# Kernel optimization log

Measured on AMD Instinct MI355X. Metric: run time of the kernel, lower is better.

Reference implementation:

```python
import jax, jax.numpy as jnp
import numpy as np
from jax import lax

WINDOW_SIZE = 11
SIGMA = 1.5
C1 = 0.01 ** 2
C2 = 0.03 ** 2


def _gaussian_window(channel, window_size=WINDOW_SIZE, sigma=SIGMA, dtype=jnp.float32):
    x = jnp.arange(window_size, dtype=dtype) - window_size // 2
    g = jnp.exp(-(x ** 2) / (2.0 * sigma ** 2))
    g = g / g.sum()
    w2 = jnp.outer(g, g)  # [K, K]
    # depthwise kernel: [C_out=C, C_in/groups=1, K, K]
    return jnp.broadcast_to(w2[None, None], (channel, 1, window_size, window_size))


def _dwconv(x, window, channel, window_size=WINDOW_SIZE):
    pad = window_size // 2
    return lax.conv_general_dilated(
        x, window,
        window_strides=(1, 1),
        padding=[(pad, pad), (pad, pad)],
        dimension_numbers=('NCHW', 'OIHW', 'NCHW'),
        feature_group_count=channel,
    )


def setup_inputs() -> dict:
    key = jax.random.key(0)
    k1, k2 = jax.random.split(key)
    img1 = jax.random.uniform(k1, (16, 3, 512, 512), dtype=jnp.float32)
    img2 = jax.random.uniform(k2, (16, 3, 512, 512), dtype=jnp.float32)
    return {"img1": img1, "img2": img2}


def reference(img1, img2):
    channel = img1.shape[1]
    window = _gaussian_window(channel, dtype=img1.dtype)

    mu1 = _dwconv(img1, window, channel)
    mu2 = _dwconv(img2, window, channel)
    mu1_sq = mu1 * mu1
    mu2_sq = mu2 * mu2
    mu1_mu2 = mu1 * mu2

    sigma1_sq = _dwconv(img1 * img1, window, channel) - mu1_sq
    sigma2_sq = _dwconv(img2 * img2, window, channel) - mu2_sq
    sigma12 = _dwconv(img1 * img2, window, channel) - mu1_mu2

    ssim_map = ((2.0 * mu1_mu2 + C1) * (2.0 * sigma12 + C2)) / (
        (mu1_sq + mu2_sq + C1) * (sigma1_sq + sigma2_sq + C2))
    return ssim_map.mean()
```

## Files before the change

kernel.cpp:

```cpp
#include <hip/hip_runtime.h>

namespace {
constexpr int IMG_W = 512, IMG_H = 512;
constexpr int TW = 32, TH = 32;
constexpr int IN_W = TW + 10, IN_H = TH + 10;
constexpr int S12_STR = 46;
constexpr float C1c = 0.01f * 0.01f;
constexpr float C2c = 0.03f * 0.03f;

constexpr float GW[11] = {
    1.0283799e-03f, 7.5987582e-03f, 3.6000773e-02f, 1.0936069e-01f,
    2.1300554e-01f, 2.6601172e-01f, 2.1300554e-01f, 1.0936069e-01f,
    3.6000773e-02f, 7.5987582e-03f, 1.0283799e-03f
};

using v2f = __attribute__((ext_vector_type(2))) float;
using v4f = __attribute__((ext_vector_type(4))) float;

__device__ __forceinline__ void pkfma(v2f& acc, v2f w, v2f a) {
    asm("v_pk_fma_f32 %0, %1, %2, %0" : "+v"(acc) : "s"(w), "v"(a));
}
__device__ __forceinline__ v2f pkmul(v2f a, v2f b) {
    v2f d;
    asm("v_pk_mul_f32 %0, %1, %2" : "=v"(d) : "v"(a), "v"(b));
    return d;
}
__device__ __forceinline__ v2f bcast(float w) { v2f r; r.x = w; r.y = w; return r; }

__device__ __forceinline__ int hidx(int row, int col) {
    return row * 32 + ((col + row) & 31);
}
}

__global__ __launch_bounds__(256, 6) void ssim_tile_kernel(
        const float* __restrict__ img1, const float* __restrict__ img2,
        double* __restrict__ acc)
{
    union SharedU {
        v2f s12[IN_H * S12_STR];
        v4f h4 [IN_H * 32];
    };
    __shared__ SharedU u;
    __shared__ float wred[4];

    const int tid = threadIdx.x;
    const size_t base = (size_t)blockIdx.z * (IMG_W * IMG_H);
    const float* p1 = img1 + base;
    const float* p2 = img2 + base;
    const int x0e = blockIdx.x * TW - 6;
    const int y0  = blockIdx.y * TH - 5;

    {
        v4f* s12v4 = (v4f*)u.s12;
        int r   = tid / 22;
        int cf2 = tid - r * 22;
        int goff = (y0 + r) * IMG_W + x0e + 2 * cf2;
        int soff = r * 23 + cf2;
        const bool interior =
            blockIdx.x > 0 && blockIdx.x < gridDim.x - 1 &&
            blockIdx.y > 0 && blockIdx.y < gridDim.y - 1;
        if (interior) {
#pragma unroll
            for (int i = 0; i < 4; ++i) {
                if (i < 3 || tid < 924 - 3 * 256) {
                    const float2 a = *(const float2*)&p1[goff];
                    const float2 b = *(const float2*)&p2[goff];
                    v4f q; q.x = a.x; q.y = b.x; q.z = a.y; q.w = b.y;
                    s12v4[soff] = q;
                }
                const bool wrap = cf2 + 14 >= 22;
                cf2  += wrap ? -8 : 14;
                r    += wrap ? 12 : 11;
                goff += wrap ? 12 * IMG_W - 16 : 11 * IMG_W + 28;
                soff += wrap ? 12 * 23 - 8     : 11 * 23 + 14;
            }
        } else {
#pragma unroll
            for (int i = 0; i < 4; ++i) {
                if (i < 3 || tid < 924 - 3 * 256) {
                    const int gy = y0 + r;
                    const int gx = x0e + 2 * cf2;
                    float a0 = 0.f, a1 = 0.f, b0 = 0.f, b1 = 0.f;
                    if (gy >= 0 && gy < IMG_H) {
                        if (gx >= 0 && gx < IMG_W)         { a0 = p1[goff];     b0 = p2[goff]; }
                        if (gx + 1 >= 0 && gx + 1 < IMG_W) { a1 = p1[goff + 1]; b1 = p2[goff + 1]; }
                    }
                    v4f q; q.x = a0; q.y = b0; q.z = a1; q.w = b1;
                    s12v4[soff] = q;
                }
                const bool wrap = cf2 + 14 >= 22;
                cf2  += wrap ? -8 : 14;
                r    += wrap ? 12 : 11;
                goff += wrap ? 12 * IMG_W - 16 : 11 * IMG_W + 28;
                soff += wrap ? 12 * 23 - 8     : 11 * 23 + 14;
            }
        }
    }
    __syncthreads();

    const int r2 = tid >> 2;
    const int g2 = tid & 3;
    const int cb = g2 * 8;
    v2f mu8[8], sx8[8];
    if (tid < 168) {
#pragma unroll
        for (int j = 0; j < 8; ++j) { mu8[j] = bcast(0.f); sx8[j] = bcast(0.f); }
        const v4f* srow = (const v4f*)u.s12 + (r2 * 23 + g2 * 4);
#pragma unroll
        for (int m = 0; m < 10; ++m) {
            const v4f q = srow[m];
#pragma unroll
            for (int half = 0; half < 2; ++half) {
                const int k = 2 * m + half;
                v2f v;
                v.x = half ? q.z : q.x;
                v.y = half ? q.w : q.y;
                const v2f a2 = pkmul(v, v);
                v2f sx;
                sx.x = a2.x + a2.y;
                sx.y = v.x * v.y;
#pragma unroll
                for (int j = 0; j < 8; ++j) {
                    const int t = k - j - 1;
                    if (t >= 0 && t < 11) {
                        const v2f w2 = bcast(GW[t]);
                        pkfma(mu8[j], w2, v);
                        pkfma(sx8[j], w2, sx);
                    }
                }
            }
        }
    }
    __syncthreads();
    if (tid < 168) {
#pragma unroll
        for (int j = 0; j < 8; ++j) {
            v4f q;
            q.x = mu8[j].x; q.y = mu8[j].y;
            q.z = sx8[j].x; q.w = sx8[j].y;
            u.h4[hidx(r2, cb + j)] = q;
        }
    }
    __syncthreads();

    const int c3 = tid & 31;
    const int rb = (tid >> 5) * 4;
    v2f mu4[4], sx4[4];
#pragma unroll
    for (int j = 0; j < 4; ++j) { mu4[j] = bcast(0.f); sx4[j] = bcast(0.f); }
#pragma unroll
    for (int k = 0; k < 14; ++k) {
        const v4f q = u.h4[hidx(rb + k, c3)];
        v2f hm; hm.x = q.x; hm.y = q.y;
        v2f hx; hx.x = q.z; hx.y = q.w;
#pragma unroll
        for (int j = 0; j < 4; ++j) {
            const int t = k - j;
            if (t >= 0 && t < 11) {
                const v2f w2 = bcast(GW[t]);
                pkfma(mu4[j], w2, hm);
                pkfma(sx4[j], w2, hx);
            }
        }
    }
    float lsum = 0.f;
#pragma unroll
    for (int j = 0; j < 4; ++j) {
        const v2f musq = pkmul(mu4[j], mu4[j]);
        const float mu12 = mu4[j].x * mu4[j].y;
        const float sden = musq.x + musq.y;
        const float s12v = sx4[j].y - mu12;
        const float ssum = sx4[j].x - sden;
        const float num = (2.f * mu12 + C1c) * (2.f * s12v + C2c);
        const float den = (sden + C1c) * (ssum + C2c);
        lsum += __fdividef(num, den);
    }

#pragma unroll
    for (int off = 32; off > 0; off >>= 1)
        lsum += __shfl_down(lsum, off, 64);
    if ((tid & 63) == 0) wred[tid >> 6] = lsum;
    __syncthreads();
    if (tid == 0) {
        const int bid = (blockIdx.z * gridDim.y + blockIdx.y) * gridDim.x + blockIdx.x;
        unsafeAtomicAdd(&acc[bid & 255],
                        (double)(wred[0] + wred[1] + wred[2] + wred[3]));
    }
}

__global__ __launch_bounds__(256) void ssim_final_kernel(
        const double* __restrict__ acc, float* __restrict__ out, double inv_total)
{
    const int tid = threadIdx.x;
    double a = acc[tid];
#pragma unroll
    for (int off = 32; off > 0; off >>= 1)
        a += __shfl_down(a, off, 64);
    __shared__ double ws[4];
    if ((tid & 63) == 0) ws[tid >> 6] = a;
    __syncthreads();
    if (tid == 0)
        out[0] = (float)((ws[0] + ws[1] + ws[2] + ws[3]) * inv_total);
}

extern "C" void kernel_launch(void* const* d_in, const int* in_sizes, int n_in,
                              void* d_out, int out_size, void* d_ws, size_t ws_size,
                              hipStream_t stream)
{
    const float* img1 = (const float*)d_in[0];
    const float* img2 = (const float*)d_in[1];
    double* acc = (double*)d_ws;

    hipMemsetAsync(d_ws, 0, 256 * sizeof(double), stream);

    const int nch = in_sizes[0] / (IMG_W * IMG_H);
    dim3 grid(IMG_W / TW, IMG_H / TH, nch);
    ssim_tile_kernel<<<grid, 256, 0, stream>>>(img1, img2, acc);

    const double inv_total = 1.0 / (double)in_sizes[0];
    ssim_final_kernel<<<1, 256, 0, stream>>>(acc, (float*)d_out, inv_total);
}
```

Baseline: 152.1 us.

## Double tile height to 64 rows and share one swizzled LDS plane

```diff
diff --git a/kernel.cpp b/kernel.cpp
--- a/kernel.cpp
+++ b/kernel.cpp
@@ -2,9 +2,10 @@
 
 namespace {
 constexpr int IMG_W = 512, IMG_H = 512;
-constexpr int TW = 32, TH = 32;
-constexpr int IN_W = TW + 10, IN_H = TH + 10;
-constexpr int S12_STR = 46;
+constexpr int TW = 32, TH = 64;
+constexpr int IN_H = TH + 10;
+constexpr int IN_UNITS = 22;
+constexpr int P1_TASKS = IN_H * IN_UNITS;
 constexpr float C1c = 0.01f * 0.01f;
 constexpr float C2c = 0.03f * 0.03f;
 
@@ -27,20 +28,16 @@
 }
 __device__ __forceinline__ v2f bcast(float w) { v2f r; r.x = w; r.y = w; return r; }
 
-__device__ __forceinline__ int hidx(int row, int col) {
+__device__ __forceinline__ int pidx(int row, int col) {
     return row * 32 + ((col + row) & 31);
 }
 }
 
-__global__ __launch_bounds__(256, 6) void ssim_tile_kernel(
+__global__ __launch_bounds__(256, 4) void ssim_tile_kernel(
         const float* __restrict__ img1, const float* __restrict__ img2,
         double* __restrict__ acc)
 {
-    union SharedU {
-        v2f s12[IN_H * S12_STR];
-        v4f h4 [IN_H * 32];
-    };
-    __shared__ SharedU u;
+    __shared__ v4f plane[IN_H * 32];
     __shared__ float wred[4];
 
     const int tid = threadIdx.x;
@@ -51,33 +48,30 @@
     const int y0  = blockIdx.y * TH - 5;
 
     {
-        v4f* s12v4 = (v4f*)u.s12;
         int r   = tid / 22;
         int cf2 = tid - r * 22;
         int goff = (y0 + r) * IMG_W + x0e + 2 * cf2;
-        int soff = r * 23 + cf2;
         const bool interior =
             blockIdx.x > 0 && blockIdx.x < gridDim.x - 1 &&
             blockIdx.y > 0 && blockIdx.y < gridDim.y - 1;
         if (interior) {
 #pragma unroll
-            for (int i = 0; i < 4; ++i) {
-                if (i < 3 || tid < 924 - 3 * 256) {
+            for (int i = 0; i < 7; ++i) {
+                if (i < 6 || tid < P1_TASKS - 6 * 256) {
                     const float2 a = *(const float2*)&p1[goff];
                     const float2 b = *(const float2*)&p2[goff];
                     v4f q; q.x = a.x; q.y = b.x; q.z = a.y; q.w = b.y;
-                    s12v4[soff] = q;
+                    plane[pidx(r, cf2)] = q;
                 }
                 const bool wrap = cf2 + 14 >= 22;
                 cf2  += wrap ? -8 : 14;
                 r    += wrap ? 12 : 11;
                 goff += wrap ? 12 * IMG_W - 16 : 11 * IMG_W + 28;
-                soff += wrap ? 12 * 23 - 8     : 11 * 23 + 14;
             }
         } else {
 #pragma unroll
-            for (int i = 0; i < 4; ++i) {
-                if (i < 3 || tid < 924 - 3 * 256) {
+            for (int i = 0; i < 7; ++i) {
+                if (i < 6 || tid < P1_TASKS - 6 * 256) {
                     const int gy = y0 + r;
                     const int gx = x0e + 2 * cf2;
                     float a0 = 0.f, a1 = 0.f, b0 = 0.f, b1 = 0.f;
@@ -86,29 +80,31 @@
                         if (gx + 1 >= 0 && gx + 1 < IMG_W) { a1 = p1[goff + 1]; b1 = p2[goff + 1]; }
                     }
                     v4f q; q.x = a0; q.y = b0; q.z = a1; q.w = b1;
-                    s12v4[soff] = q;
+                    plane[pidx(r, cf2)] = q;
                 }
                 const bool wrap = cf2 + 14 >= 22;
                 cf2  += wrap ? -8 : 14;
                 r    += wrap ? 12 : 11;
                 goff += wrap ? 12 * IMG_W - 16 : 11 * IMG_W + 28;
-                soff += wrap ? 12 * 23 - 8     : 11 * 23 + 14;
-            }
-        }
-    }
-    __syncthreads();
-
-    const int r2 = tid >> 2;
-    const int g2 = tid & 3;
-    const int cb = g2 * 8;
-    v2f mu8[8], sx8[8];
-    if (tid < 168) {
+            }
+        }
+    }
+    __syncthreads();
+
+    v2f muA[8], sxA[8], muB[8], sxB[8];
+    const int rA = tid >> 2;
+    const int gA = tid & 3;
+    const bool hasB = tid < 40;
+    const int rB = 64 + (tid >> 2);
+
+    auto hconv = [&](int r2, int g2, v2f* mu8, v2f* sx8) {
 #pragma unroll
         for (int j = 0; j < 8; ++j) { mu8[j] = bcast(0.f); sx8[j] = bcast(0.f); }
-        const v4f* srow = (const v4f*)u.s12 + (r2 * 23 + g2 * 4);
+        const int rowb = r2 * 32;
+        const int cb   = g2 * 4 + r2;
 #pragma unroll
         for (int m = 0; m < 10; ++m) {
-            const v4f q = srow[m];
+            const v4f q = plane[rowb + ((cb + m) & 31)];
 #pragma unroll
             for (int half = 0; half < 2; ++half) {
                 const int k = 2 * m + half;
@@ -130,47 +126,57 @@
                 }
             }
         }
-    }
-    __syncthreads();
-    if (tid < 168) {
+    };
+
+    hconv(rA, gA, muA, sxA);
+    if (hasB) hconv(rB, gA, muB, sxB);
+    __syncthreads();
+#pragma unroll
+    for (int j = 0; j < 8; ++j) {
+        v4f q;
+        q.x = muA[j].x; q.y = muA[j].y;
+        q.z = sxA[j].x; q.w = sxA[j].y;
+        plane[pidx(rA, 8 * gA + j)] = q;
+    }
+    if (hasB) {
 #pragma unroll
         for (int j = 0; j < 8; ++j) {
             v4f q;
-            q.x = mu8[j].x; q.y = mu8[j].y;
-            q.z = sx8[j].x; q.w = sx8[j].y;
-            u.h4[hidx(r2, cb + j)] = q;
+            q.x = muB[j].x; q.y = muB[j].y;
+            q.z = sxB[j].x; q.w = sxB[j].y;
+            plane[pidx(rB, 8 * gA + j)] = q;
         }
     }
     __syncthreads();
 
     const int c3 = tid & 31;
-    const int rb = (tid >> 5) * 4;
-    v2f mu4[4], sx4[4];
-#pragma unroll
-    for (int j = 0; j < 4; ++j) { mu4[j] = bcast(0.f); sx4[j] = bcast(0.f); }
-#pragma unroll
-    for (int k = 0; k < 14; ++k) {
-        const v4f q = u.h4[hidx(rb + k, c3)];
+    const int rb = (tid >> 5) * 8;
+    v2f mu8[8], sx8[8];
+#pragma unroll
+    for (int j = 0; j < 8; ++j) { mu8[j] = bcast(0.f); sx8[j] = bcast(0.f); }
+#pragma unroll
+    for (int k = 0; k < 18; ++k) {
+        const v4f q = plane[pidx(rb + k, c3)];
         v2f hm; hm.x = q.x; hm.y = q.y;
         v2f hx; hx.x = q.z; hx.y = q.w;
 #pragma unroll
-        for (int j = 0; j < 4; ++j) {
+        for (int j = 0; j < 8; ++j) {
             const int t = k - j;
             if (t >= 0 && t < 11) {
                 const v2f w2 = bcast(GW[t]);
-                pkfma(mu4[j], w2, hm);
-                pkfma(sx4[j], w2, hx);
+                pkfma(mu8[j], w2, hm);
+                pkfma(sx8[j], w2, hx);
             }
         }
     }
     float lsum = 0.f;
 #pragma unroll
-    for (int j = 0; j < 4; ++j) {
-        const v2f musq = pkmul(mu4[j], mu4[j]);
-        const float mu12 = mu4[j].x * mu4[j].y;
+    for (int j = 0; j < 8; ++j) {
+        const v2f musq = pkmul(mu8[j], mu8[j]);
+        const float mu12 = mu8[j].x * mu8[j].y;
         const float sden = musq.x + musq.y;
-        const float s12v = sx4[j].y - mu12;
-        const float ssum = sx4[j].x - sden;
+        const float s12v = sx8[j].y - mu12;
+        const float ssum = sx8[j].x - sden;
         const float num = (2.f * mu12 + C1c) * (2.f * s12v + C2c);
         const float den = (sden + C1c) * (ssum + C2c);
         lsum += __fdividef(num, den);
```

New measurement: 160.0 us. 1.05x slower.
